# Kernel tuning notes

Hardware: AMD Instinct MI355X
Metric: run time of the kernel (lower is better)

## Reference

```python
import jax, jax.numpy as jnp
import numpy as np

B, N, M, K = 8, 9225, 4096, 32
D = 2          # coordinate dim
HID = 64       # MLP hidden
DOUT = 16      # MLP output / f_y channels


def setup_inputs() -> dict:
    key = jax.random.key(0)
    ks = jax.random.split(key, 10)
    y = jax.random.uniform(ks[0], (B, N, D), dtype=jnp.float32)
    x = jax.random.uniform(ks[1], (B, M, D), dtype=jnp.float32)
    f_y = jax.random.uniform(ks[2], (B, N, DOUT), dtype=jnp.float32)
    weights = jax.random.uniform(ks[3], (B, N), dtype=jnp.float32)
    neighbors_index = jax.random.randint(ks[4], (B, M, K), 0, N, dtype=jnp.int64)
    drop = jax.random.uniform(ks[5], (B, M, K)) < 0.1
    neighbors_index = jnp.where(drop, jnp.int64(-1), neighbors_index)
    # LinearChannelMLP params: 4 -> 64 -> 16, gelu between
    W1 = jax.random.normal(ks[6], (2 * D, HID), dtype=jnp.float32) * (1.0 / np.sqrt(2 * D))
    b1 = jnp.zeros((HID,), dtype=jnp.float32)
    W2 = jax.random.normal(ks[7], (HID, DOUT), dtype=jnp.float32) * (1.0 / np.sqrt(HID))
    b2 = jnp.zeros((DOUT,), dtype=jnp.float32)
    return {"y": y, "x": x, "f_y": f_y, "weights": weights,
            "W1": W1, "b1": b1, "W2": W2, "b2": b2,
            "neighbors_index": neighbors_index}


def _batched_gather(table, idx):
    # table: [B, N, ...], idx: [B, M, K] -> [B, M, K, ...]
    return jax.vmap(lambda t, i: t[i])(table, idx)


def reference(y, x, f_y, weights, W1, b1, W2, b2, neighbors_index):
    idx = jnp.where(neighbors_index == -1, 0, neighbors_index)      # [B,M,K]
    valid = (neighbors_index != -1).astype(y.dtype)[..., None]      # [B,M,K,1]

    rep_y = _batched_gather(y, idx)                                 # [B,M,K,D]
    in_f = _batched_gather(f_y, idx)                                # [B,M,K,DOUT]
    self_x = jnp.broadcast_to(x[:, :, None, :], rep_y.shape)        # [B,M,K,D]

    agg = jnp.concatenate([rep_y, self_x], axis=-1)                 # [B,M,K,2D]
    h = jax.nn.gelu(agg @ W1 + b1, approximate=False)               # [B,M,K,HID]
    kval = h @ W2 + b2                                              # [B,M,K,DOUT]

    kval = kval * in_f                                              # linear transform: k(x,y)*f(y)
    w_nbr = _batched_gather(weights, idx)[..., None]                # [B,M,K,1]
    kval = kval * w_nbr * valid
    return kval.sum(axis=2)                                         # [B,M,DOUT]
```

## Files before the change

### kernel.cpp

```cpp
#include <hip/hip_runtime.h>
#include <hip/hip_bf16.h>

#define B_    8
#define N_    9225
#define M_    4096
#define K_    32
#define HID_  64
#define DOUT_ 16

typedef __attribute__((ext_vector_type(8))) short short8;
typedef __attribute__((ext_vector_type(4))) float floatx4;
typedef __attribute__((ext_vector_type(2))) float f32x2;

static __device__ __forceinline__ short f2bf(float f) {
    __hip_bfloat16 h = __float2bfloat16(f);
    return __builtin_bit_cast(short, h);
}
static __device__ __forceinline__ float bf2f(short s) {
    unsigned u = ((unsigned)(unsigned short)s) << 16;
    return __builtin_bit_cast(float, u);
}
static __device__ __forceinline__ f32x2 splat2(float v) { return (f32x2){v, v}; }

static __device__ __forceinline__ float row16_sum(float v) {
    int t;
    t = __builtin_amdgcn_update_dpp(0, __builtin_bit_cast(int, v), 0x111, 0xF, 0xF, true);
    v += __builtin_bit_cast(float, t);
    t = __builtin_amdgcn_update_dpp(0, __builtin_bit_cast(int, v), 0x112, 0xF, 0xF, true);
    v += __builtin_bit_cast(float, t);
    t = __builtin_amdgcn_update_dpp(0, __builtin_bit_cast(int, v), 0x114, 0xF, 0xF, true);
    v += __builtin_bit_cast(float, t);
    t = __builtin_amdgcn_update_dpp(0, __builtin_bit_cast(int, v), 0x118, 0xF, 0xF, true);
    v += __builtin_bit_cast(float, t);
    return v;
}

static __device__ __forceinline__ f32x2 gelu2(f32x2 x) {
    const f32x2 xsq = x * x;
    const f32x2 t   = __builtin_elementwise_fma(xsq, splat2(0.035677408f), splat2(0.79788456f));
    const f32x2 z   = x * t;
    const f32x2 u   = z * z;
    const f32x2 a   = u + splat2(105.0f);
    const f32x2 nin = __builtin_elementwise_fma(u, a, splat2(945.0f));
    const f32x2 num = z * nin;
    const f32x2 bq  = __builtin_elementwise_fma(u, splat2(15.0f), splat2(420.0f));
    const f32x2 den = __builtin_elementwise_fma(u, bq, splat2(945.0f));
    const f32x2 r   = { __builtin_amdgcn_rcpf(den[0]), __builtin_amdgcn_rcpf(den[1]) };
    f32x2 th = num * r;
    th = __builtin_elementwise_min(__builtin_elementwise_max(th, splat2(-1.0f)), splat2(1.0f));
    const f32x2 hx = x * splat2(0.5f);
    return __builtin_elementwise_fma(hx, th, hx);
}

__global__ __launch_bounds__(256, 4) void it_kernel(
    const float* __restrict__ y,
    const float* __restrict__ x,
    const float* __restrict__ f_y,
    const float* __restrict__ weights,
    const float* __restrict__ W1,
    const float* __restrict__ b1,
    const float* __restrict__ W2,
    const float* __restrict__ b2,
    const int*   __restrict__ nbr,
    float*       __restrict__ out)
{
    __shared__ float b1L[64];
    __shared__ float b2L[16];

    const int tid = threadIdx.x;
    if (tid < 64) b1L[tid] = b1[tid];
    if (tid < 16) b2L[tid] = b2[tid];

    const int lane = tid & 63;
    const int q    = lane >> 4;
    const int nlo  = lane & 15;

    const int blk   = blockIdx.x;
    const int batch = blk & 7;
    const int pblk  = blk >> 3;
    const int wid   = tid >> 6;
    const int row0  = __builtin_amdgcn_readfirstlane(batch * M_ + pblk * 16 + wid * 4);
    const int bbase = batch * N_;

    short8 w1h[4];
    #pragma unroll
    for (int t = 0; t < 4; ++t) {
        #pragma unroll
        for (int jj = 0; jj < 8; ++jj) w1h[t][jj] = 0;
        #pragma unroll
        for (int jj = 0; jj < 4; ++jj) {
            const float wv = W1[jj * HID_ + t * 16 + nlo];
            w1h[t][jj] = (q == 0) ? f2bf(wv) : (short)0;
        }
    }

    short8 w2f[2];
    #pragma unroll
    for (int ch = 0; ch < 2; ++ch)
        #pragma unroll
        for (int jj = 0; jj < 8; ++jj) {
            const int H = (ch * 2 + (jj >> 2)) * 16 + q * 4 + (jj & 3);
            w2f[ch][jj] = f2bf(W2[H * DOUT_ + nlo]);
        }

    short xh[8], xl[8];
    #pragma unroll
    for (int it = 0; it < 4; ++it) {
        const float2 xv = *(const float2*)(x + (size_t)(row0 + it) * 2);
        const short h0 = f2bf(xv.x); const short l0 = f2bf(xv.x - bf2f(h0));
        const short h1 = f2bf(xv.y); const short l1 = f2bf(xv.y - bf2f(h1));
        xh[it * 2] = h0; xh[it * 2 + 1] = h1;
        xl[it * 2] = l0; xl[it * 2 + 1] = l1;
    }

    int raw[8];
    #pragma unroll
    for (int ph = 0; ph < 8; ++ph) {
        const int it = ph >> 1, h = ph & 1;
        raw[ph] = nbr[(size_t)(row0 + it) * K_ + h * 16 + nlo];
    }

    float2 yv[8]; float sw[8]; floatx4 fv[8];
    #define GATH(P) { \
        const int rv  = raw[P]; \
        const int vld = rv >= 0; \
        const int bn  = bbase + (vld ? rv : 0); \
        yv[P] = *(const float2*)(y + (size_t)bn * 2); \
        const float wv_ = weights[bn]; \
        sw[P] = vld ? wv_ : 0.0f; \
        fv[P] = *(const floatx4*)(f_y + (size_t)bn * DOUT_ + q * 4); \
    }
    GATH(0); GATH(1);

    __syncthreads();

    float partial[4] = {0.f, 0.f, 0.f, 0.f};
    #pragma unroll
    for (int ph = 0; ph < 8; ++ph) {
        if (ph + 2 < 8) GATH(ph + 2);
        const int it = ph >> 1;

        const float y0 = yv[ph].x, y1 = yv[ph].y;
        const short yh0 = f2bf(y0); const short yl0 = f2bf(y0 - bf2f(yh0));
        const short yh1 = f2bf(y1); const short yl1 = f2bf(y1 - bf2f(yh1));
        const bool q0 = (q == 0);
        const short z = 0;
        const short8 bhi = { q0 ? yh0 : z, q0 ? yh1 : z,
                             q0 ? xh[it * 2] : z, q0 ? xh[it * 2 + 1] : z,
                             z, z, z, z };
        const short8 blo = { q0 ? yl0 : z, q0 ? yl1 : z,
                             q0 ? xl[it * 2] : z, q0 ? xl[it * 2 + 1] : z,
                             z, z, z, z };

        floatx4 a1[4];
        #pragma unroll
        for (int t = 0; t < 4; ++t) {
            a1[t] = *(const floatx4*)&b1L[t * 16 + q * 4];
            a1[t] = __builtin_amdgcn_mfma_f32_16x16x32_bf16(w1h[t], bhi, a1[t], 0, 0, 0);
            a1[t] = __builtin_amdgcn_mfma_f32_16x16x32_bf16(w1h[t], blo, a1[t], 0, 0, 0);
        }

        short hv[16];
        #pragma unroll
        for (int t = 0; t < 4; ++t) {
            const f32x2 g01 = gelu2((f32x2){a1[t][0], a1[t][1]});
            const f32x2 g23 = gelu2((f32x2){a1[t][2], a1[t][3]});
            hv[t * 4 + 0] = f2bf(g01[0]); hv[t * 4 + 1] = f2bf(g01[1]);
            hv[t * 4 + 2] = f2bf(g23[0]); hv[t * 4 + 3] = f2bf(g23[1]);
        }
        const short8 hf0 = {hv[0], hv[1], hv[2],  hv[3],  hv[4],  hv[5],  hv[6],  hv[7]};
        const short8 hf1 = {hv[8], hv[9], hv[10], hv[11], hv[12], hv[13], hv[14], hv[15]};

        floatx4 acc = *(const floatx4*)&b2L[q * 4];
        acc = __builtin_amdgcn_mfma_f32_16x16x32_bf16(w2f[0], hf0, acc, 0, 0, 0);
        acc = __builtin_amdgcn_mfma_f32_16x16x32_bf16(w2f[1], hf1, acc, 0, 0, 0);

        const floatx4 fvp = fv[ph];
        const float   s   = sw[ph];
        #pragma unroll
        for (int r = 0; r < 4; ++r)
            partial[r] = fmaf(acc[r], fvp[r] * s, partial[r]);

        if (ph & 1) {
            #pragma unroll
            for (int r = 0; r < 4; ++r) partial[r] = row16_sum(partial[r]);
            if (nlo == 15) {
                floatx4 o = {partial[0], partial[1], partial[2], partial[3]};
                *(floatx4*)(out + (size_t)(row0 + it) * DOUT_ + q * 4) = o;
            }
            #pragma unroll
            for (int r = 0; r < 4; ++r) partial[r] = 0.f;
        }
    }
    #undef GATH
}

extern "C" void kernel_launch(void* const* d_in, const int* in_sizes, int n_in,
                              void* d_out, int out_size, void* d_ws, size_t ws_size,
                              hipStream_t stream) {
    const float* y   = (const float*)d_in[0];
    const float* x   = (const float*)d_in[1];
    const float* f_y = (const float*)d_in[2];
    const float* w   = (const float*)d_in[3];
    const float* W1  = (const float*)d_in[4];
    const float* b1  = (const float*)d_in[5];
    const float* W2  = (const float*)d_in[6];
    const float* b2  = (const float*)d_in[7];
    const int*   nbr = (const int*)d_in[8];
    float* out = (float*)d_out;

    dim3 grid(B_ * M_ / 16), block(256);
    hipLaunchKernelGGL(it_kernel, grid, block, 0, stream,
                       y, x, f_y, w, W1, b1, W2, b2, nbr, out);
}
```

Measured before the change: 108.7 us.

## Pack y and weights into float4 table, merge hi/lo MFMAs, deepen gather prefetch

Adds a pre-pass kernel that packs y coordinates and per-point weights into one 16-byte record per point, so each neighbour gather needs one y/weight load instead of two. The first-layer MFMA now carries the hi and lo bf16 halves in one K-slot, halving layer-1 MFMA count. Biases move from LDS into registers, which drops the __syncthreads. Gather prefetch depth grows from 2 to 4 phases. The costs are an extra kernel launch, a workspace write/read pass, and higher register pressure from the deeper prefetch.

```diff
diff --git a/kernel.cpp b/kernel.cpp
--- a/kernel.cpp
+++ b/kernel.cpp
@@ -52,6 +52,17 @@
     return __builtin_elementwise_fma(hx, th, hx);
 }
 
+__global__ __launch_bounds__(256) void pack_yw(
+    const float* __restrict__ y, const float* __restrict__ w,
+    floatx4* __restrict__ ywp)
+{
+    const int i = blockIdx.x * 256 + threadIdx.x;
+    if (i < B_ * N_) {
+        const float2 yv = *(const float2*)(y + (size_t)i * 2);
+        ywp[i] = (floatx4){yv.x, yv.y, w[i], 0.0f};
+    }
+}
+
 __global__ __launch_bounds__(256, 4) void it_kernel(
     const float* __restrict__ y,
     const float* __restrict__ x,
@@ -62,18 +73,15 @@
     const float* __restrict__ W2,
     const float* __restrict__ b2,
     const int*   __restrict__ nbr,
+    const floatx4* __restrict__ ywp,
+    const int    packed,
     float*       __restrict__ out)
 {
-    __shared__ float b1L[64];
-    __shared__ float b2L[16];
-
-    const int tid = threadIdx.x;
-    if (tid < 64) b1L[tid] = b1[tid];
-    if (tid < 16) b2L[tid] = b2[tid];
-
+    const int tid  = threadIdx.x;
     const int lane = tid & 63;
     const int q    = lane >> 4;
     const int nlo  = lane & 15;
+    const bool q0  = (q == 0);
 
     const int blk   = blockIdx.x;
     const int batch = blk & 7;
@@ -86,11 +94,11 @@
     #pragma unroll
     for (int t = 0; t < 4; ++t) {
         #pragma unroll
-        for (int jj = 0; jj < 8; ++jj) w1h[t][jj] = 0;
-        #pragma unroll
         for (int jj = 0; jj < 4; ++jj) {
             const float wv = W1[jj * HID_ + t * 16 + nlo];
-            w1h[t][jj] = (q == 0) ? f2bf(wv) : (short)0;
+            const short b  = q0 ? f2bf(wv) : (short)0;
+            w1h[t][jj]     = b;
+            w1h[t][jj + 4] = b;
         }
     }
 
@@ -102,6 +110,12 @@
             const int H = (ch * 2 + (jj >> 2)) * 16 + q * 4 + (jj & 3);
             w2f[ch][jj] = f2bf(W2[H * DOUT_ + nlo]);
         }
+
+    floatx4 b1r[4];
+    #pragma unroll
+    for (int t = 0; t < 4; ++t)
+        b1r[t] = *(const floatx4*)(b1 + t * 16 + q * 4);
+    const floatx4 b2r = *(const floatx4*)(b2 + q * 4);
 
     short xh[8], xl[8];
     #pragma unroll
@@ -120,44 +134,37 @@
         raw[ph] = nbr[(size_t)(row0 + it) * K_ + h * 16 + nlo];
     }
 
-    float2 yv[8]; float sw[8]; floatx4 fv[8];
+    floatx4 ywv[8]; floatx4 fv[8];
     #define GATH(P) { \
         const int rv  = raw[P]; \
-        const int vld = rv >= 0; \
-        const int bn  = bbase + (vld ? rv : 0); \
-        yv[P] = *(const float2*)(y + (size_t)bn * 2); \
-        const float wv_ = weights[bn]; \
-        sw[P] = vld ? wv_ : 0.0f; \
+        const int bn  = bbase + (rv >= 0 ? rv : 0); \
+        if (packed) { \
+            ywv[P] = ywp[bn]; \
+        } else { \
+            const float2 y2 = *(const float2*)(y + (size_t)bn * 2); \
+            ywv[P] = (floatx4){y2.x, y2.y, weights[bn], 0.0f}; \
+        } \
         fv[P] = *(const floatx4*)(f_y + (size_t)bn * DOUT_ + q * 4); \
     }
-    GATH(0); GATH(1);
-
-    __syncthreads();
+    GATH(0); GATH(1); GATH(2); GATH(3);
 
     float partial[4] = {0.f, 0.f, 0.f, 0.f};
     #pragma unroll
     for (int ph = 0; ph < 8; ++ph) {
-        if (ph + 2 < 8) GATH(ph + 2);
+        if (ph + 4 < 8) GATH(ph + 4);
         const int it = ph >> 1;
 
-        const float y0 = yv[ph].x, y1 = yv[ph].y;
+        const float y0 = ywv[ph][0], y1 = ywv[ph][1];
         const short yh0 = f2bf(y0); const short yl0 = f2bf(y0 - bf2f(yh0));
         const short yh1 = f2bf(y1); const short yl1 = f2bf(y1 - bf2f(yh1));
-        const bool q0 = (q == 0);
-        const short z = 0;
-        const short8 bhi = { q0 ? yh0 : z, q0 ? yh1 : z,
-                             q0 ? xh[it * 2] : z, q0 ? xh[it * 2 + 1] : z,
-                             z, z, z, z };
-        const short8 blo = { q0 ? yl0 : z, q0 ? yl1 : z,
-                             q0 ? xl[it * 2] : z, q0 ? xl[it * 2 + 1] : z,
-                             z, z, z, z };
+        const short8 bfull = { yh0, yh1, xh[it * 2], xh[it * 2 + 1],
+                               yl0, yl1, xl[it * 2], xl[it * 2 + 1] };
 
         floatx4 a1[4];
         #pragma unroll
         for (int t = 0; t < 4; ++t) {
-            a1[t] = *(const floatx4*)&b1L[t * 16 + q * 4];
-            a1[t] = __builtin_amdgcn_mfma_f32_16x16x32_bf16(w1h[t], bhi, a1[t], 0, 0, 0);
-            a1[t] = __builtin_amdgcn_mfma_f32_16x16x32_bf16(w1h[t], blo, a1[t], 0, 0, 0);
+            a1[t] = b1r[t];
+            a1[t] = __builtin_amdgcn_mfma_f32_16x16x32_bf16(w1h[t], bfull, a1[t], 0, 0, 0);
         }
 
         short hv[16];
@@ -171,12 +178,12 @@
         const short8 hf0 = {hv[0], hv[1], hv[2],  hv[3],  hv[4],  hv[5],  hv[6],  hv[7]};
         const short8 hf1 = {hv[8], hv[9], hv[10], hv[11], hv[12], hv[13], hv[14], hv[15]};
 
-        floatx4 acc = *(const floatx4*)&b2L[q * 4];
+        floatx4 acc = b2r;
         acc = __builtin_amdgcn_mfma_f32_16x16x32_bf16(w2f[0], hf0, acc, 0, 0, 0);
         acc = __builtin_amdgcn_mfma_f32_16x16x32_bf16(w2f[1], hf1, acc, 0, 0, 0);
 
         const floatx4 fvp = fv[ph];
-        const float   s   = sw[ph];
+        const float   s   = (raw[ph] >= 0) ? ywv[ph][2] : 0.0f;
         #pragma unroll
         for (int r = 0; r < 4; ++r)
             partial[r] = fmaf(acc[r], fvp[r] * s, partial[r]);
@@ -209,7 +216,15 @@
     const int*   nbr = (const int*)d_in[8];
     float* out = (float*)d_out;
 
+    const size_t need = (size_t)B_ * N_ * 16;
+    const int packed = (d_ws != nullptr && ws_size >= need) ? 1 : 0;
+    floatx4* ywp = (floatx4*)d_ws;
+    if (packed) {
+        dim3 pgrid((B_ * N_ + 255) / 256), pblock(256);
+        hipLaunchKernelGGL(pack_yw, pgrid, pblock, 0, stream, y, w, ywp);
+    }
+
     dim3 grid(B_ * M_ / 16), block(256);
     hipLaunchKernelGGL(it_kernel, grid, block, 0, stream,
-                       y, x, f_y, w, W1, b1, W2, b2, nbr, out);
-}
+                       y, x, f_y, w, W1, b1, W2, b2, nbr, ywp, packed, out);
+}
```

Result: no change. 107.8 us (-0.8%).
